# Optimization experiments

Hardware: AMD Instinct MI355X
Metric: run time of the kernel (lower is better)

The kernel has to match this reference:

```python
import jax, jax.numpy as jnp
import numpy as np

NEG_INF = -1e9  # stands in for the eye(W)*sys.maxsize self-mask on the row axis


def setup_inputs() -> dict:
    key = jax.random.key(0)
    ks = jax.random.split(key, 8)
    B, C, S = 8, 512, 128
    C8 = C // 8
    sc = 0.02
    x = jax.random.normal(ks[0], (B, C, S, S), dtype=jnp.float32)
    Wq = jax.random.normal(ks[1], (C8, C), dtype=jnp.float32) * sc
    bq = jnp.zeros((C8,), dtype=jnp.float32)
    Wk = jax.random.normal(ks[2], (C8, C), dtype=jnp.float32) * sc
    bk = jnp.zeros((C8,), dtype=jnp.float32)
    Wv = jax.random.normal(ks[3], (C, C), dtype=jnp.float32) * sc
    bv = jnp.zeros((C,), dtype=jnp.float32)
    gamma = jnp.ones((1,), dtype=jnp.float32) * 0.5  # source inits to 0; nonzero so path is exercised
    return {"x": x, "Wq": Wq, "bq": bq, "Wk": Wk, "bk": bk, "Wv": Wv, "bv": bv, "gamma": gamma}


def reference(x, Wq, bq, Wk, bk, Wv, bv, gamma):
    # x: (B, C, W, H) with W == H == S (required by the eye-mask view in the source)
    B, C, S, _ = x.shape
    # 1x1 convs = per-pixel linear projections
    q = jnp.einsum('oc,bcwh->bowh', Wq, x) + bq[None, :, None, None]  # (B,C8,S,S)
    k = jnp.einsum('oc,bcwh->bowh', Wk, x) + bk[None, :, None, None]
    v = jnp.einsum('oc,bcwh->bowh', Wv, x) + bv[None, :, None, None]  # (B,C,S,S)

    # column ('h'-fixed) attention along W, self position masked out
    e_col = jnp.einsum('bcwh,bcuh->bwhu', q, k)  # (B,W,H,W)
    self_mask = jnp.eye(S, dtype=bool)  # w == u
    e_col = jnp.where(self_mask[None, :, None, :], NEG_INF, e_col)
    # row ('w'-fixed) attention along H
    e_row = jnp.einsum('bcwh,bcwu->bwhu', q, k)  # (B,W,H,H)

    att = jax.nn.softmax(jnp.concatenate([e_col, e_row], axis=-1), axis=-1)  # (B,W,H,2S)
    a_col = att[..., :S]   # weights over w'
    a_row = att[..., S:]   # weights over h'

    out = (jnp.einsum('bwhu,bcuh->bcwh', a_col, v)
           + jnp.einsum('bwhu,bcwu->bcwh', a_row, v))  # (B,C,S,S)
    return gamma[0] * out + x
```

## Files before the change

### kernel.cpp

```cpp
#include <hip/hip_runtime.h>
#include <hip/hip_bf16.h>


#define S 128
#define SS 16384
#define C 512
#define C8 64
#define NEG_BIG -1000000000.0f

using short8 = __attribute__((ext_vector_type(8))) short;
using f32x4  = __attribute__((ext_vector_type(4))) float;

#define GPTR(p) ((const __attribute__((address_space(1))) void*)(p))
#define LPTR(p) ((__attribute__((address_space(3))) void*)(p))

#define PR(r) ((((r) & 7) << 4) | ((r) >> 3))

__device__ __forceinline__ unsigned short f2b(float f){
  union { float f; unsigned u; } v; v.f = f;
  unsigned r = (v.u + 0x7fffu + ((v.u >> 16) & 1u)) >> 16;
  return (unsigned short)r;
}
__device__ __forceinline__ float b2f(unsigned short h){
  union { unsigned u; float f; } v; v.u = ((unsigned)h) << 16;
  return v.f;
}

template<int NT>
__device__ __forceinline__ void stage_tile64(unsigned short* dst,
    const unsigned short* src, size_t rstride, int tid){
  #pragma unroll
  for (int p = 0; p < 1024 / NT; ++p){
    int gi = p * NT + tid;
    int row = gi >> 3, cc = gi & 7;
    int kc = (cc ^ (row & 7)) * 8;
    __builtin_amdgcn_global_load_lds(GPTR(src + (size_t)row * rstride + kc),
                                     LPTR((char*)dst + gi * 16), 16, 0, 0);
  }
}

__global__ __launch_bounds__(256) void k_xp_pack(
    const float* __restrict__ x, unsigned short* __restrict__ xp,
    const float* __restrict__ Wq, const float* __restrict__ Wk,
    const float* __restrict__ Wv, unsigned short* __restrict__ wall){
  __shared__ unsigned short T[128 * 130] __attribute__((aligned(16)));
  int blk = blockIdx.x;
  if (blk >= 4096){
    int i = (blk - 4096) * 256 + threadIdx.x;
    int co = i >> 9, ci = i & (C - 1);
    float v;
    if (co < 64)        v = Wq[co * C + ci];
    else if (co < 128)  v = Wk[(co - 64) * C + ci];
    else                v = Wv[(co - 128) * C + ci];
    wall[i] = f2b(v);
    return;
  }
  int ct = blk & 3; int bw = blk >> 2;
  int w = bw & 127; int b = bw >> 7;
  int tid = threadIdx.x;
  int ci0 = ct * 128;
  const float* xb = x + ((size_t)(b * C + ci0) * S + w) * S;
  #pragma unroll
  for (int p = 0; p < 16; ++p){
    int idx = p * 256 + tid;
    int cc = idx >> 5;
    int h4 = (idx & 31) * 4;
    float4 v = *(const float4*)(xb + (size_t)cc * SS + h4);
    unsigned* d = (unsigned*)&T[PR(cc) * 130 + h4];
    d[0] = (unsigned)f2b(v.x) | ((unsigned)f2b(v.y) << 16);
    d[1] = (unsigned)f2b(v.z) | ((unsigned)f2b(v.w) << 16);
  }
  __syncthreads();
  unsigned short* xpb = xp + (size_t)(b * S + w) * S * C + ci0;
  #pragma unroll
  for (int p = 0; p < 8; ++p){
    int idx = p * 256 + tid;
    int h  = idx >> 4;
    int ch = (idx & 15) * 8;
    unsigned short tmp[8] __attribute__((aligned(16)));
    #pragma unroll
    for (int j = 0; j < 8; ++j) tmp[j] = T[PR(ch + j) * 130 + h];
    *(uint4*)(xpb + (size_t)h * C + ch) = *(uint4*)tmp;
  }
}

__global__ __launch_bounds__(256) void k_qkv(
    const unsigned short* __restrict__ xp, const unsigned short* __restrict__ wall,
    const float* __restrict__ bq, const float* __restrict__ bk,
    const float* __restrict__ bv,
    unsigned short* __restrict__ qp, unsigned short* __restrict__ kp,
    unsigned short* __restrict__ vb){
  __shared__ unsigned short sm[24576] __attribute__((aligned(16)));
  unsigned short* Dl = sm;
  int blk = blockIdx.x;
  int pxsub = blk & 7; int t = blk >> 3;
  int cot = t % 5; int pxg = t / 5;
  int pxt = pxg * 8 + pxsub;
  int w = pxt & 127, b = pxt >> 7;
  int tid = threadIdx.x, lane = tid & 63, wid = tid >> 6;
  int qd = lane >> 4, ln = lane & 15;
  const unsigned short* asrc0 = wall + (size_t)cot * 128 * C;
  const unsigned short* bsrc0 = xp + (size_t)pxt * 128 * C;
  const unsigned short* arow[4];
  #pragma unroll
  for (int i = 0; i < 4; ++i)
    arow[i] = asrc0 + (size_t)(((wid & 1) * 4 + i) * 16 + ln) * C + qd * 8;
  f32x4 acc[4][4];
  #pragma unroll
  for (int i = 0; i < 4; ++i)
    #pragma unroll
    for (int j = 0; j < 4; ++j) acc[i][j] = (f32x4){0.f, 0.f, 0.f, 0.f};
  short8 afr[2][2][4];

  stage_tile64<256>(sm,        bsrc0,      C, tid);
  stage_tile64<256>(sm + 8192, bsrc0 + 64, C, tid);
  #pragma unroll
  for (int ks = 0; ks < 2; ++ks)
    #pragma unroll
    for (int i = 0; i < 4; ++i)
      afr[0][ks][i] = *(const short8*)(arow[i] + ks * 32);

  #pragma unroll
  for (int kw = 0; kw < 8; ++kw){
    if (kw < 7) asm volatile("s_waitcnt vmcnt(12)" ::: "memory");
    else        asm volatile("s_waitcnt vmcnt(0)"  ::: "memory");
    __builtin_amdgcn_s_barrier();
    if (kw < 7){
      #pragma unroll
      for (int ks = 0; ks < 2; ++ks)
        #pragma unroll
        for (int i = 0; i < 4; ++i)
          afr[(kw + 1) & 1][ks][i] =
            *(const short8*)(arow[i] + (kw + 1) * 64 + ks * 32);
    }
    if (kw < 6)
      stage_tile64<256>(sm + ((kw + 2) % 3) * 8192,
                        bsrc0 + (kw + 2) * 64, C, tid);
    const unsigned short* Bl = sm + (kw % 3) * 8192;
    __builtin_amdgcn_s_setprio(1);
    #pragma unroll
    for (int ks = 0; ks < 2; ++ks){
      int ch8 = (((ks * 4 + qd) ^ (ln & 7)) * 8);
      short8 bfr[4];
      #pragma unroll
      for (int j = 0; j < 4; ++j)
        bfr[j] = *(const short8*)&Bl[(((wid >> 1) * 4 + j) * 16 + ln) * 64 + ch8];
      #pragma unroll
      for (int i = 0; i < 4; ++i)
        #pragma unroll
        for (int j = 0; j < 4; ++j)
          acc[i][j] = __builtin_amdgcn_mfma_f32_16x16x32_bf16(afr[kw & 1][ks][i], bfr[j], acc[i][j], 0, 0, 0);
    }
    __builtin_amdgcn_s_setprio(0);
  }
  __syncthreads();
  float bias_[4][4];
  #pragma unroll
  for (int i = 0; i < 4; ++i){
    int co_l0 = ((wid & 1) * 4 + i) * 16 + qd * 4;
    #pragma unroll
    for (int r = 0; r < 4; ++r){
      int co_l = co_l0 + r;
      bias_[i][r] = (cot == 0) ? (co_l < 64 ? bq[co_l] : bk[co_l - 64])
                               : bv[(cot - 1) * 128 + co_l];
    }
  }
  #pragma unroll
  for (int i = 0; i < 4; ++i){
    int co_l0 = ((wid & 1) * 4 + i) * 16 + qd * 4;
    #pragma unroll
    for (int j = 0; j < 4; ++j){
      int pxl = ((wid >> 1) * 4 + j) * 16 + ln;
      #pragma unroll
      for (int r = 0; r < 4; ++r)
        Dl[(co_l0 + r) * 136 + pxl] = f2b(acc[i][j][r] + bias_[i][r]);
    }
  }
  __syncthreads();
  if (cot == 0){
    unsigned short* qb = qp + (size_t)(b * S + w) * S * C8;
    unsigned short* kb = kp + (size_t)(b * S + w) * S * C8;
    #pragma unroll
    for (int p = 0; p < 4; ++p){
      int idx = p * 256 + tid;
      int cch = idx & 7, hh = idx >> 3;
      unsigned short tq[8] __attribute__((aligned(16)));
      unsigned short tk[8] __attribute__((aligned(16)));
      #pragma unroll
      for (int jj = 0; jj < 8; ++jj){
        tq[jj] = Dl[(cch * 8 + jj) * 136 + hh];
        tk[jj] = Dl[(64 + cch * 8 + jj) * 136 + hh];
      }
      *(uint4*)(qb + (size_t)hh * C8 + cch * 8) = *(uint4*)tq;
      *(uint4*)(kb + (size_t)hh * C8 + cch * 8) = *(uint4*)tk;
    }
  } else {
    unsigned short* vbb = vb + ((size_t)(b * C + (cot - 1) * 128) * S + w) * S;
    #pragma unroll
    for (int p = 0; p < 8; ++p){
      int idx = p * 256 + tid;
      int c_l = idx >> 4, hc = (idx & 15) * 8;
      uint4 v = *(const uint4*)&Dl[c_l * 136 + hc];
      *(uint4*)(vbb + (size_t)c_l * SS + hc) = v;
    }
  }
}

__global__ __launch_bounds__(256) void k_tv_ecol(
    const unsigned short* __restrict__ vb, unsigned short* __restrict__ vt,
    const unsigned short* __restrict__ qp, const unsigned short* __restrict__ kp,
    unsigned short* __restrict__ eca){
  __shared__ char smu[36864] __attribute__((aligned(16)));
  int blk = blockIdx.x;
  int tid = threadIdx.x;
  if (blk < 4096){
    unsigned short* T = (unsigned short*)smu;
    const unsigned short* src = vb + (size_t)blk * SS;
    unsigned short* dst = vt + (size_t)blk * SS;
    #pragma unroll
    for (int p = 0; p < 8; ++p){
      int idx = p * 256 + tid;
      int wv = idx >> 4, ch = (idx & 15) * 8;
      uint4 v = *(const uint4*)(src + wv * S + ch);
      unsigned* d = (unsigned*)&T[PR(wv) * 130 + ch];
      d[0] = v.x; d[1] = v.y; d[2] = v.z; d[3] = v.w;
    }
    __syncthreads();
    #pragma unroll
    for (int p = 0; p < 8; ++p){
      int idx = p * 256 + tid;
      int h = idx >> 4, ch = (idx & 15) * 8;
      unsigned short tmp[8] __attribute__((aligned(16)));
      #pragma unroll
      for (int j = 0; j < 8; ++j) tmp[j] = T[PR(ch + j) * 130 + h];
      *(uint4*)(dst + h * S + ch) = *(uint4*)tmp;
    }
    return;
  }
  unsigned short* Aq = (unsigned short*)smu;
  unsigned short* Bk = (unsigned short*)(smu + 18432);
  int e = blk - 4096; int h = e & 127, b = e >> 7;
  int lane = tid & 63, wid = tid >> 6;
  int qd = lane >> 4, ln = lane & 15;
  #pragma unroll
  for (int p = 0; p < 4; ++p){
    int idx = p * 256 + tid;
    int row = idx >> 3, ch = (idx & 7) * 8;
    *(uint4*)&Aq[row * 72 + ch] = *(const uint4*)(qp + ((size_t)(b * S + row) * S + h) * C8 + ch);
    *(uint4*)&Bk[row * 72 + ch] = *(const uint4*)(kp + ((size_t)(b * S + row) * S + h) * C8 + ch);
  }
  __syncthreads();
  f32x4 acc[4][4];
  #pragma unroll
  for (int i = 0; i < 4; ++i)
    #pragma unroll
    for (int j = 0; j < 4; ++j) acc[i][j] = (f32x4){0.f, 0.f, 0.f, 0.f};
  #pragma unroll
  for (int ks = 0; ks < 2; ++ks){
    int ko = ks * 32 + qd * 8;
    short8 af[4], bfr[4];
    #pragma unroll
    for (int i = 0; i < 4; ++i)
      af[i] = *(const short8*)&Aq[(((wid & 1) * 4 + i) * 16 + ln) * 72 + ko];
    #pragma unroll
    for (int j = 0; j < 4; ++j)
      bfr[j] = *(const short8*)&Bk[(((wid >> 1) * 4 + j) * 16 + ln) * 72 + ko];
    #pragma unroll
    for (int i = 0; i < 4; ++i)
      #pragma unroll
      for (int j = 0; j < 4; ++j)
        acc[i][j] = __builtin_amdgcn_mfma_f32_16x16x32_bf16(af[i], bfr[j], acc[i][j], 0, 0, 0);
  }
  #pragma unroll
  for (int i = 0; i < 4; ++i){
    int w0 = (((wid & 1) * 4 + i) * 16) + qd * 4;
    #pragma unroll
    for (int j = 0; j < 4; ++j){
      int ug = ((wid >> 1) * 4 + j) * 16 + ln;
      #pragma unroll
      for (int r = 0; r < 4; ++r){
        int wg = w0 + r;
        float val = acc[i][j][r];
        if (wg == ug) val = NEG_BIG;
        eca[((size_t)(b * S + wg) * S + h) * S + ug] = f2b(val);
      }
    }
  }
}

__global__ __launch_bounds__(256) void k_erow_sm_outrow(
    const unsigned short* __restrict__ qp, const unsigned short* __restrict__ kp,
    unsigned short* __restrict__ eca, unsigned short* vb){
  __shared__ char sm[71680] __attribute__((aligned(16)));
  unsigned short* Aq  = (unsigned short*)sm;
  unsigned short* Bk  = (unsigned short*)(sm + 18432);
  unsigned short* El  = (unsigned short*)sm;
  unsigned short* Av0 = (unsigned short*)(sm + 36864);
  unsigned short* Av1 = (unsigned short*)(sm + 53248);
  float* redm = (float*)(sm + 69632);
  float* reds = (float*)(sm + 70656);
  int blk = blockIdx.x; int w = blk & 127, b = blk >> 7;
  int tid = threadIdx.x, lane = tid & 63, wid = tid >> 6;
  int qd = lane >> 4, ln = lane & 15;
  size_t tb = (size_t)(b * S + w) * SS;
  const unsigned short* vsrc0 = vb + (size_t)(b * C) * SS + (size_t)w * S;

  {
    const unsigned short* qsrc = qp + (size_t)(b * S + w) * S * C8;
    const unsigned short* ksrc = kp + (size_t)(b * S + w) * S * C8;
    #pragma unroll
    for (int p = 0; p < 4; ++p){
      int idx = p * 256 + tid;
      int row = idx >> 3, ch = (idx & 7) * 8;
      *(uint4*)&Aq[row * 72 + ch] = *(const uint4*)(qsrc + row * C8 + ch);
      *(uint4*)&Bk[row * 72 + ch] = *(const uint4*)(ksrc + row * C8 + ch);
    }
  }
  stage_tile64<256>(Av0, vsrc0, SS, tid);
  __syncthreads();
  f32x4 acc[4][4];
  #pragma unroll
  for (int i = 0; i < 4; ++i)
    #pragma unroll
    for (int j = 0; j < 4; ++j) acc[i][j] = (f32x4){0.f, 0.f, 0.f, 0.f};
  #pragma unroll
  for (int ks = 0; ks < 2; ++ks){
    int ko = ks * 32 + qd * 8;
    short8 af[4], bfr[4];
    #pragma unroll
    for (int i = 0; i < 4; ++i)
      af[i] = *(const short8*)&Aq[(((wid & 1) * 4 + i) * 16 + ln) * 72 + ko];
    #pragma unroll
    for (int j = 0; j < 4; ++j)
      bfr[j] = *(const short8*)&Bk[(((wid >> 1) * 4 + j) * 16 + ln) * 72 + ko];
    #pragma unroll
    for (int i = 0; i < 4; ++i)
      #pragma unroll
      for (int j = 0; j < 4; ++j)
        acc[i][j] = __builtin_amdgcn_mfma_f32_16x16x32_bf16(af[i], bfr[j], acc[i][j], 0, 0, 0);
  }
  __syncthreads();
  #pragma unroll
  for (int i = 0; i < 4; ++i){
    int h0 = ((wid & 1) * 4 + i) * 16 + qd * 4;
    #pragma unroll
    for (int j = 0; j < 4; ++j){
      int ul = ((wid >> 1) * 4 + j) * 16 + ln;
      #pragma unroll
      for (int r = 0; r < 4; ++r)
        El[(h0 + r) * 136 + ul] = f2b(acc[i][j][r]);
    }
  }
  __syncthreads();
  {
    int h = tid >> 1, half = tid & 1;
    const uint4* src4 = (half == 0) ? (const uint4*)(eca + tb + (size_t)h * S)
                                    : (const uint4*)&El[h * 136];
    float mx = -3.0e38f;
    #pragma unroll 4
    for (int u = 0; u < 16; ++u){
      uint4 v = src4[u];
      const unsigned short* e = (const unsigned short*)&v;
      #pragma unroll
      for (int jj = 0; jj < 8; ++jj) mx = fmaxf(mx, b2f(e[jj]));
    }
    redm[tid] = mx;
    __syncthreads();
    float m = fmaxf(mx, redm[tid ^ 1]);
    float s = 0.f;
    #pragma unroll 4
    for (int u = 0; u < 16; ++u){
      uint4 v = src4[u];
      const unsigned short* e = (const unsigned short*)&v;
      #pragma unroll
      for (int jj = 0; jj < 8; ++jj) s += __expf(b2f(e[jj]) - m);
    }
    reds[tid] = s;
    __syncthreads();
    float inv = 1.0f / (s + reds[tid ^ 1]);
    uint4* dst4 = (half == 0) ? (uint4*)(eca + tb + (size_t)h * S)
                              : (uint4*)&El[h * 136];
    #pragma unroll 4
    for (int u = 0; u < 16; ++u){
      uint4 v = src4[u];
      const unsigned short* e = (const unsigned short*)&v;
      unsigned short o[8] __attribute__((aligned(16)));
      #pragma unroll
      for (int jj = 0; jj < 8; ++jj) o[jj] = f2b(__expf(b2f(e[jj]) - m) * inv);
      dst4[u] = *(uint4*)o;
    }
  }
  __syncthreads();

  for (int s = 0; s < 8; ++s){
    int ct = s >> 1, kw = s & 1;
    unsigned short* Acur = (s & 1) ? Av1 : Av0;
    if (s < 7){
      int ct1 = (s + 1) >> 1, kw1 = (s + 1) & 1;
      stage_tile64<256>((s & 1) ? Av0 : Av1,
                        vsrc0 + (size_t)(ct1 * 128) * SS + kw1 * 64, SS, tid);
    }
    if (kw == 0){
      #pragma unroll
      for (int i = 0; i < 4; ++i)
        #pragma unroll
        for (int j = 0; j < 4; ++j) acc[i][j] = (f32x4){0.f, 0.f, 0.f, 0.f};
    }
    __builtin_amdgcn_s_setprio(1);
    #pragma unroll
    for (int ks = 0; ks < 2; ++ks){
      int ch8 = (((ks * 4 + qd) ^ (ln & 7)) * 8);
      int ko = kw * 64 + ks * 32 + qd * 8;
      short8 af[4], bfr[4];
      #pragma unroll
      for (int i = 0; i < 4; ++i)
        af[i] = *(const short8*)&Acur[(((wid & 1) * 4 + i) * 16 + ln) * 64 + ch8];
      #pragma unroll
      for (int j = 0; j < 4; ++j)
        bfr[j] = *(const short8*)&El[(((wid >> 1) * 4 + j) * 16 + ln) * 136 + ko];
      #pragma unroll
      for (int i = 0; i < 4; ++i)
        #pragma unroll
        for (int j = 0; j < 4; ++j)
          acc[i][j] = __builtin_amdgcn_mfma_f32_16x16x32_bf16(af[i], bfr[j], acc[i][j], 0, 0, 0);
    }
    __builtin_amdgcn_s_setprio(0);
    if (kw == 1){
      #pragma unroll
      for (int i = 0; i < 4; ++i){
        int c0 = ((wid & 1) * 4 + i) * 16 + qd * 4;
        #pragma unroll
        for (int j = 0; j < 4; ++j){
          int hl = ((wid >> 1) * 4 + j) * 16 + ln;
          #pragma unroll
          for (int r = 0; r < 4; ++r){
            int cg = ct * 128 + c0 + r;
            vb[((size_t)(b * C + cg) * S + w) * S + hl] = f2b(acc[i][j][r]);
          }
        }
      }
    }
    __syncthreads();
  }
}

__global__ __launch_bounds__(256) void k_outcol(
    const unsigned short* __restrict__ vt, const unsigned short* __restrict__ eca,
    unsigned short* __restrict__ oct){
  __shared__ unsigned short Av[128 * 72] __attribute__((aligned(16)));
  __shared__ unsigned short Ba[128 * 72] __attribute__((aligned(16)));
  int blk = blockIdx.x;
  int ct = blk & 3; int bh = blk >> 2;
  int h = bh & 127, b = bh >> 7;
  int tid = threadIdx.x, lane = tid & 63, wid = tid >> 6;
  int qd = lane >> 4, ln = lane & 15;
  f32x4 acc[4][4];
  #pragma unroll
  for (int i = 0; i < 4; ++i)
    #pragma unroll
    for (int j = 0; j < 4; ++j) acc[i][j] = (f32x4){0.f, 0.f, 0.f, 0.f};
  for (int kw = 0; kw < 2; ++kw){
    __syncthreads();
    #pragma unroll
    for (int p = 0; p < 4; ++p){
      int idx = p * 256 + tid;
      int row = idx >> 3, ch = (idx & 7) * 8;
      *(uint4*)&Av[row * 72 + ch] =
        *(const uint4*)(vt + ((size_t)(b * C + ct * 128 + row) * S + h) * S + kw * 64 + ch);
      *(uint4*)&Ba[row * 72 + ch] =
        *(const uint4*)(eca + ((size_t)(b * S + row) * S + h) * S + kw * 64 + ch);
    }
    __syncthreads();
    #pragma unroll
    for (int ks = 0; ks < 2; ++ks){
      int ko = ks * 32 + qd * 8;
      short8 af[4], bfr[4];
      #pragma unroll
      for (int i = 0; i < 4; ++i)
        af[i] = *(const short8*)&Av[(((wid & 1) * 4 + i) * 16 + ln) * 72 + ko];
      #pragma unroll
      for (int j = 0; j < 4; ++j)
        bfr[j] = *(const short8*)&Ba[(((wid >> 1) * 4 + j) * 16 + ln) * 72 + ko];
      #pragma unroll
      for (int i = 0; i < 4; ++i)
        #pragma unroll
        for (int j = 0; j < 4; ++j)
          acc[i][j] = __builtin_amdgcn_mfma_f32_16x16x32_bf16(af[i], bfr[j], acc[i][j], 0, 0, 0);
    }
  }
  #pragma unroll
  for (int i = 0; i < 4; ++i){
    int c0 = ((wid & 1) * 4 + i) * 16 + qd * 4;
    #pragma unroll
    for (int j = 0; j < 4; ++j){
      int wl = ((wid >> 1) * 4 + j) * 16 + ln;
      #pragma unroll
      for (int r = 0; r < 4; ++r){
        int cg = ct * 128 + c0 + r;
        oct[((size_t)(b * S + h) * C + cg) * S + wl] = f2b(acc[i][j][r]);
      }
    }
  }
}

__global__ __launch_bounds__(256) void k_final(
    const unsigned short* __restrict__ oct, const unsigned short* __restrict__ orw,
    const float* __restrict__ x, const float* __restrict__ gamma,
    float* __restrict__ out){
  __shared__ unsigned short T[128 * 130] __attribute__((aligned(16)));
  int blk = blockIdx.x;
  int c = blk & 511, b = blk >> 9;
  int tid = threadIdx.x;
  float g = gamma[0];
  #pragma unroll
  for (int p = 0; p < 8; ++p){
    int idx = p * 256 + tid;
    int hh = idx >> 4, ch = (idx & 15) * 8;
    uint4 v = *(const uint4*)(oct + ((size_t)(b * S + hh) * C + c) * S + ch);
    unsigned* d = (unsigned*)&T[PR(hh) * 130 + ch];
    d[0] = v.x; d[1] = v.y; d[2] = v.z; d[3] = v.w;
  }
  __syncthreads();
  #pragma unroll
  for (int p = 0; p < 8; ++p){
    int idx = p * 256 + tid;
    int wv = idx >> 4, hch = (idx & 15) * 8;
    size_t o = ((size_t)(b * C + c) * S + wv) * S + hch;
    uint4 rv = *(const uint4*)(orw + o);
    const unsigned short* rr = (const unsigned short*)&rv;
    float4 x0 = *(const float4*)(x + o);
    float4 x1 = *(const float4*)(x + o + 4);
    float4 o0, o1;
    o0.x = g * (b2f(rr[0]) + b2f(T[PR(hch + 0) * 130 + wv])) + x0.x;
    o0.y = g * (b2f(rr[1]) + b2f(T[PR(hch + 1) * 130 + wv])) + x0.y;
    o0.z = g * (b2f(rr[2]) + b2f(T[PR(hch + 2) * 130 + wv])) + x0.z;
    o0.w = g * (b2f(rr[3]) + b2f(T[PR(hch + 3) * 130 + wv])) + x0.w;
    o1.x = g * (b2f(rr[4]) + b2f(T[PR(hch + 4) * 130 + wv])) + x1.x;
    o1.y = g * (b2f(rr[5]) + b2f(T[PR(hch + 5) * 130 + wv])) + x1.y;
    o1.z = g * (b2f(rr[6]) + b2f(T[PR(hch + 6) * 130 + wv])) + x1.z;
    o1.w = g * (b2f(rr[7]) + b2f(T[PR(hch + 7) * 130 + wv])) + x1.w;
    *(float4*)(out + o) = o0;
    *(float4*)(out + o + 4) = o1;
  }
}

extern "C" void kernel_launch(void* const* d_in, const int* in_sizes, int n_in,
                              void* d_out, int out_size, void* d_ws, size_t ws_size,
                              hipStream_t stream){
  const float* x     = (const float*)d_in[0];
  const float* Wq    = (const float*)d_in[1];
  const float* bq    = (const float*)d_in[2];
  const float* Wk    = (const float*)d_in[3];
  const float* bk    = (const float*)d_in[4];
  const float* Wv    = (const float*)d_in[5];
  const float* bv    = (const float*)d_in[6];
  const float* gamma = (const float*)d_in[7];
  float* out = (float*)d_out;
  char* ws = (char*)d_ws;

  const size_t OFF_WALL = 0;
  const size_t OFF_XP   = 1ull << 20;
  const size_t OFF_QP   = OFF_XP  + 134217728ull;
  const size_t OFF_KP   = OFF_QP  + 16777216ull;
  const size_t OFF_VB   = OFF_KP  + 16777216ull;
  const size_t OFF_VT   = OFF_VB  + 134217728ull;
  const size_t OFF_ECA  = OFF_VT  + 134217728ull;
  const size_t OFF_OCT  = OFF_XP;
  const size_t NEED     = OFF_ECA + 33554432ull;
  if (ws_size < NEED) return;

  unsigned short* wall = (unsigned short*)(ws + OFF_WALL);
  unsigned short* xp   = (unsigned short*)(ws + OFF_XP);
  unsigned short* qp   = (unsigned short*)(ws + OFF_QP);
  unsigned short* kp   = (unsigned short*)(ws + OFF_KP);
  unsigned short* vb   = (unsigned short*)(ws + OFF_VB);
  unsigned short* vt   = (unsigned short*)(ws + OFF_VT);
  unsigned short* eca  = (unsigned short*)(ws + OFF_ECA);
  unsigned short* oct  = (unsigned short*)(ws + OFF_OCT);

  k_xp_pack       <<<5376, 256, 0, stream>>>(x, xp, Wq, Wk, Wv, wall);
  k_qkv           <<<5120, 256, 0, stream>>>(xp, wall, bq, bk, bv, qp, kp, vb);
  k_tv_ecol       <<<5120, 256, 0, stream>>>(vb, vt, qp, kp, eca);
  k_erow_sm_outrow<<<1024, 256, 0, stream>>>(qp, kp, eca, vb);
  k_outcol        <<<4096, 256, 0, stream>>>(vt, eca, oct);
  k_final         <<<4096, 256, 0, stream>>>(oct, vb, x, gamma, out);
}
```

Baseline: 990.2 us.

## Stage weight tiles through LDS in qkv GEMM and relayout oct buffer

The qkv projection kernel now stages both the weight (A) and activation (B) operands into LDS as 32-wide K tiles with XOR swizzling, using a triple-buffered pipeline of 16 K-steps. Previously the weights were read straight from global memory into registers. This is meant to cut redundant global weight traffic and register pressure, at the cost of more barriers and smaller K chunks per step. Separately, the column-attention output buffer is stored as (b,c,h,w) instead of (b,h,c,w), so the final kernel reads one contiguous 32 KB block per channel rather than strided rows.

```diff
diff --git a/kernel.cpp b/kernel.cpp
--- a/kernel.cpp
+++ b/kernel.cpp
@@ -35,6 +35,18 @@
     int row = gi >> 3, cc = gi & 7;
     int kc = (cc ^ (row & 7)) * 8;
     __builtin_amdgcn_global_load_lds(GPTR(src + (size_t)row * rstride + kc),
+                                     LPTR((char*)dst + gi * 16), 16, 0, 0);
+  }
+}
+
+__device__ __forceinline__ void stage_tile32(unsigned short* dst,
+    const unsigned short* src, int tid){
+  #pragma unroll
+  for (int p = 0; p < 2; ++p){
+    int gi = p * 256 + tid;
+    int row = gi >> 2, cc = gi & 3;
+    int kc = (cc ^ ((row >> 1) & 3)) * 8;
+    __builtin_amdgcn_global_load_lds(GPTR(src + (size_t)row * C + kc),
                                      LPTR((char*)dst + gi * 16), 16, 0, 0);
   }
 }
@@ -101,56 +113,47 @@
   int qd = lane >> 4, ln = lane & 15;
   const unsigned short* asrc0 = wall + (size_t)cot * 128 * C;
   const unsigned short* bsrc0 = xp + (size_t)pxt * 128 * C;
-  const unsigned short* arow[4];
+  int offA[4], offB[4];
+  #pragma unroll
+  for (int i = 0; i < 4; ++i){
+    int Ra = ((wid & 1) * 4 + i) * 16 + ln;
+    offA[i] = Ra * 32 + ((qd ^ ((Ra >> 1) & 3)) * 8);
+    int Rb = ((wid >> 1) * 4 + i) * 16 + ln;
+    offB[i] = Rb * 32 + ((qd ^ ((Rb >> 1) & 3)) * 8) + 4096;
+  }
+  f32x4 acc[4][4];
   #pragma unroll
   for (int i = 0; i < 4; ++i)
-    arow[i] = asrc0 + (size_t)(((wid & 1) * 4 + i) * 16 + ln) * C + qd * 8;
-  f32x4 acc[4][4];
-  #pragma unroll
-  for (int i = 0; i < 4; ++i)
     #pragma unroll
     for (int j = 0; j < 4; ++j) acc[i][j] = (f32x4){0.f, 0.f, 0.f, 0.f};
-  short8 afr[2][2][4];
-
-  stage_tile64<256>(sm,        bsrc0,      C, tid);
-  stage_tile64<256>(sm + 8192, bsrc0 + 64, C, tid);
-  #pragma unroll
-  for (int ks = 0; ks < 2; ++ks)
-    #pragma unroll
-    for (int i = 0; i < 4; ++i)
-      afr[0][ks][i] = *(const short8*)(arow[i] + ks * 32);
-
-  #pragma unroll
-  for (int kw = 0; kw < 8; ++kw){
-    if (kw < 7) asm volatile("s_waitcnt vmcnt(12)" ::: "memory");
-    else        asm volatile("s_waitcnt vmcnt(0)"  ::: "memory");
+
+  stage_tile32(sm,        asrc0,      tid);
+  stage_tile32(sm + 4096, bsrc0,      tid);
+  stage_tile32(sm + 8192,        asrc0 + 32, tid);
+  stage_tile32(sm + 8192 + 4096, bsrc0 + 32, tid);
+
+  #pragma unroll
+  for (int kw = 0; kw < 16; ++kw){
+    if (kw < 15) asm volatile("s_waitcnt vmcnt(4)" ::: "memory");
+    else         asm volatile("s_waitcnt vmcnt(0)" ::: "memory");
     __builtin_amdgcn_s_barrier();
-    if (kw < 7){
-      #pragma unroll
-      for (int ks = 0; ks < 2; ++ks)
-        #pragma unroll
-        for (int i = 0; i < 4; ++i)
-          afr[(kw + 1) & 1][ks][i] =
-            *(const short8*)(arow[i] + (kw + 1) * 64 + ks * 32);
-    }
-    if (kw < 6)
-      stage_tile64<256>(sm + ((kw + 2) % 3) * 8192,
-                        bsrc0 + (kw + 2) * 64, C, tid);
+    if (kw < 14){
+      unsigned short* nb = sm + ((kw + 2) % 3) * 8192;
+      stage_tile32(nb,        asrc0 + (kw + 2) * 32, tid);
+      stage_tile32(nb + 4096, bsrc0 + (kw + 2) * 32, tid);
+    }
     const unsigned short* Bl = sm + (kw % 3) * 8192;
     __builtin_amdgcn_s_setprio(1);
-    #pragma unroll
-    for (int ks = 0; ks < 2; ++ks){
-      int ch8 = (((ks * 4 + qd) ^ (ln & 7)) * 8);
-      short8 bfr[4];
+    short8 af[4], bfr[4];
+    #pragma unroll
+    for (int i = 0; i < 4; ++i) af[i]  = *(const short8*)&Bl[offA[i]];
+    #pragma unroll
+    for (int j = 0; j < 4; ++j) bfr[j] = *(const short8*)&Bl[offB[j]];
+    #pragma unroll
+    for (int i = 0; i < 4; ++i)
       #pragma unroll
       for (int j = 0; j < 4; ++j)
-        bfr[j] = *(const short8*)&Bl[(((wid >> 1) * 4 + j) * 16 + ln) * 64 + ch8];
-      #pragma unroll
-      for (int i = 0; i < 4; ++i)
-        #pragma unroll
-        for (int j = 0; j < 4; ++j)
-          acc[i][j] = __builtin_amdgcn_mfma_f32_16x16x32_bf16(afr[kw & 1][ks][i], bfr[j], acc[i][j], 0, 0, 0);
-    }
+        acc[i][j] = __builtin_amdgcn_mfma_f32_16x16x32_bf16(af[i], bfr[j], acc[i][j], 0, 0, 0);
     __builtin_amdgcn_s_setprio(0);
   }
   __syncthreads();
@@ -497,7 +500,7 @@
       #pragma unroll
       for (int r = 0; r < 4; ++r){
         int cg = ct * 128 + c0 + r;
-        oct[((size_t)(b * S + h) * C + cg) * S + wl] = f2b(acc[i][j][r]);
+        oct[((size_t)(b * C + cg) * S + h) * S + wl] = f2b(acc[i][j][r]);
       }
     }
   }
@@ -512,11 +515,12 @@
   int c = blk & 511, b = blk >> 9;
   int tid = threadIdx.x;
   float g = gamma[0];
+  const unsigned short* osrc = oct + (size_t)(b * C + c) * SS;
   #pragma unroll
   for (int p = 0; p < 8; ++p){
     int idx = p * 256 + tid;
     int hh = idx >> 4, ch = (idx & 15) * 8;
-    uint4 v = *(const uint4*)(oct + ((size_t)(b * S + hh) * C + c) * S + ch);
+    uint4 v = *(const uint4*)(osrc + hh * S + ch);
     unsigned* d = (unsigned*)&T[PR(hh) * 130 + ch];
     d[0] = v.x; d[1] = v.y; d[2] = v.z; d[3] = v.w;
   }
```

Result: faster. 923.0 us (-6.8%).
